# Optimization experiments

Hardware: AMD Instinct MI355X
Metric: run time of the kernel (lower is better)

The kernel has to match this reference:

```python
import jax, jax.numpy as jnp
from jax import lax
import numpy as np

H = 512        # hidden_state_dim
D = 300        # embedding dim (data.x.shape[1])
VG = 40000     # n globals = last_idx_globals - last_idx_senses
VS = 25000     # n senses  = last_idx_senses
NNODES = 65000 # rows of X (senses + globals)
T = 1024       # flattened token sequence length


def setup_inputs() -> dict:
    key = jax.random.key(0)
    ks = jax.random.split(key, 18)
    s = 0.05
    w = lambda k, shape: (jax.random.normal(k, shape, jnp.float32) * s)
    return {
        "tokens": jax.random.randint(ks[0], (T,), 0, NNODES),
        "X":   w(ks[1], (NNODES, D)),
        "Wz1": w(ks[2], (D, H)), "Uz1": w(ks[3], (H, H)),
        "Wr1": w(ks[4], (D, H)), "Ur1": w(ks[5], (H, H)),
        "W1":  w(ks[6], (D, H)), "U1":  w(ks[7], (H, H)),
        "Wz2": w(ks[8], (H, H)), "Uz2": w(ks[9], (H, H)),
        "Wr2": w(ks[10], (H, H)), "Ur2": w(ks[11], (H, H)),
        "W2":  w(ks[12], (H, H)), "U2":  w(ks[13], (H, H)),
        "Wg":  w(ks[14], (H, VG)), "bg": jnp.zeros((VG,), jnp.float32),
        "Ws":  w(ks[15], (H, VS)), "bs": jnp.zeros((VS,), jnp.float32),
    }


def reference(tokens, X, Wz1, Uz1, Wr1, Ur1, W1, U1,
              Wz2, Uz2, Wr2, Ur2, W2, U2, Wg, bg, Ws, bs):
    # Embedding gather for the whole sequence up front (same math as
    # per-step index_select). Dropout (p=0.1) treated as eval/identity.
    x_emb = X[tokens]                       # [T, D]
    h = Uz1.shape[0]
    h0 = jnp.zeros((h,), X.dtype)

    def step(carry, x):
        h1, h2 = carry
        # layer-1 GRU cell
        z1 = jax.nn.sigmoid(x @ Wz1 + h1 @ Uz1)
        r1 = jax.nn.sigmoid(x @ Wr1 + h1 @ Ur1)
        ht1 = jnp.tanh(x @ W1 + (r1 * h1) @ U1)
        h1n = z1 * ht1 + (1.0 - z1) * h1
        # layer-2 GRU cell
        z2 = jax.nn.sigmoid(h1n @ Wz2 + h2 @ Uz2)
        r2 = jax.nn.sigmoid(h1n @ Wr2 + h2 @ Ur2)
        ht2 = jnp.tanh(h1n @ W2 + (r2 * h2) @ U2)
        h2n = z2 * ht2 + (1.0 - z2) * h2
        return (h1n, h2n), h2n

    _, h2s = lax.scan(step, (h0, h0), x_emb)   # h2s: [T, H]

    # vocab projections + log-softmax, batched over all tokens
    pred_globals = jax.nn.log_softmax(h2s @ Wg + bg, axis=-1)  # [T, VG]
    pred_senses = jax.nn.log_softmax(h2s @ Ws + bs, axis=-1)   # [T, VS]
    return pred_globals, pred_senses
```

## Files before the change

### kernel.cpp

```cpp
#include <hip/hip_runtime.h>
#include <stdint.h>

typedef unsigned short u16;
typedef unsigned int u32;
typedef unsigned long long u64;

#define Hdim 512
#define Ddim 300
#define Tlen 1024
#define VG 40000
#define VS 25000
#define NGTOT (Tlen * VG)
#define NTOT  (Tlen * (VG + VS))

#define F_XZ   0
#define F_XR   (F_XZ + Tlen * Hdim)
#define F_X1   (F_XR + Tlen * Hdim)
#define F_H1X  (F_X1 + Tlen * Hdim)
#define F_H2X  (F_H1X + (Tlen + 1) * Hdim * 2)
#define F_R1X  (F_H2X + (Tlen + 1) * Hdim * 2)
#define F_R2X  (F_R1X + Tlen * Hdim * 2)
#define F_HBF  (F_R2X + Tlen * Hdim * 2)
#define F_WGBF (F_HBF + (Tlen * Hdim) / 2)
#define F_WSBF (F_WGBF + (Hdim * VG) / 2)
#define F_PG   (F_WSBF + (Hdim * VS) / 2)
#define F_PS   (F_PG + Tlen * 625)
#define F_LSE  (F_PS + Tlen * 391)

__device__ __forceinline__ u16 f2bf(float f) {
    u32 u = __float_as_uint(f);
    u += 0x7fffu + ((u >> 16) & 1u);
    return (u16)(u >> 16);
}
__device__ __forceinline__ float bf2f(u16 s) { return __uint_as_float(((u32)s) << 16); }
__device__ __forceinline__ float sigm(float x) { return 1.f / (1.f + __expf(-x)); }

__device__ __forceinline__ u64 pk(u32 tag, float v) {
    return ((u64)tag << 32) | (u64)__float_as_uint(v);
}
__device__ __forceinline__ float upf(u64 x) { return __uint_as_float((u32)x); }
__device__ __forceinline__ u32 uptag(u64 x) { return (u32)(x >> 32); }
__device__ __forceinline__ u64 ld64(const u64* p) {
    return __hip_atomic_load(p, __ATOMIC_RELAXED, __HIP_MEMORY_SCOPE_AGENT);
}
__device__ __forceinline__ void st64(u64* p, u64 v) {
    __hip_atomic_store(p, v, __ATOMIC_RELAXED, __HIP_MEMORY_SCOPE_AGENT);
}
__device__ __forceinline__ u64 spin64(const u64* p, u32 tg) {
    u64 a = ld64(p);
    while (uptag(a) != tg) { __builtin_amdgcn_s_sleep(1); a = ld64(p); }
    return a;
}

__global__ void k_init(u64* h1x, u64* h2x) {
    int i = blockIdx.x * 256 + threadIdx.x;
    if (i < Hdim) { h1x[i] = pk(1u, 0.f); h2x[i] = pk(1u, 0.f); }
}

__launch_bounds__(256)
__global__ void k_xproj(const int* tokens, const float* X,
                        const float* Wz1, const float* Wr1, const float* W1,
                        float* xz, float* xr, float* x1) {
    int tid = threadIdx.x;
    int jj = tid & 63, tg = tid >> 6;
    int mat = blockIdx.y >> 3;
    int j0 = (blockIdx.y & 7) * 64;
    int t0 = blockIdx.x * 16 + tg * 4;
    const float* W = (mat == 0) ? Wz1 : (mat == 1 ? Wr1 : W1);
    float* out = (mat == 0) ? xz : (mat == 1 ? xr : x1);
    const float* xrow[4];
#pragma unroll
    for (int u = 0; u < 4; ++u) xrow[u] = X + (size_t)tokens[t0 + u] * Ddim;
    float acc[4] = {0.f, 0.f, 0.f, 0.f};
    for (int k = 0; k < Ddim; ++k) {
        float w = W[(size_t)k * Hdim + j0 + jj];
#pragma unroll
        for (int u = 0; u < 4; ++u) acc[u] += xrow[u][k] * w;
    }
#pragma unroll
    for (int u = 0; u < 4; ++u) out[(size_t)(t0 + u) * Hdim + j0 + jj] = acc[u];
}

__global__ void k_wconv(const float* Wg, const float* Ws, u16* wgbf, u16* wsbf) {
    const int n4g = (Hdim * VG) / 4;
    const int n4s = (Hdim * VS) / 4;
    int stride = gridDim.x * blockDim.x;
    for (int i = blockIdx.x * blockDim.x + threadIdx.x; i < n4g + n4s; i += stride) {
        float4 v;
        u64* dst;
        if (i < n4g) { v = ((const float4*)Wg)[i]; dst = (u64*)wgbf + i; }
        else { int j = i - n4g; v = ((const float4*)Ws)[j]; dst = (u64*)wsbf + j; }
        u64 p = (u64)f2bf(v.x) | ((u64)f2bf(v.y) << 16) | ((u64)f2bf(v.z) << 32) | ((u64)f2bf(v.w) << 48);
        *dst = p;
    }
}

__global__ void k_hbf(const u64* h2x, u16* hbf) {
    int i = blockIdx.x * 256 + threadIdx.x;
    hbf[i] = f2bf(upf(ld64(&h2x[i + Hdim])));
}

#define G1n 32
#define C1n 16
#define G2n 64
#define C2n 8
#define WS 516

__launch_bounds__(256)
__global__ void k_scan(const float* Uz1, const float* Ur1, const float* U1,
                       const float* Wz2, const float* Uz2, const float* Wr2,
                       const float* Ur2, const float* W2, const float* U2,
                       const float* xz, const float* xr, const float* x1,
                       u64* h1x, u64* h2x, u64* r1x, u64* r2x) {
    __shared__ u16 wsl[48 * WS];
    __shared__ float hA[2][Hdim], hB[2][Hdim], hC[2][Hdim];
    int tid = threadIdx.x;
    int g = blockIdx.x;

    if (g < G1n) {
        int c0 = g * C1n;
        const float* Us[3] = {Uz1, Ur1, U1};
        for (int m = 0; m < 3; ++m) {
            for (int k = 0; k < 2; ++k) {
                int i = tid + k * 256;
                const float* src = Us[m] + (size_t)i * Hdim + c0;
                float v[16];
#pragma unroll
                for (int q = 0; q < 4; ++q) {
                    float4 f = ((const float4*)src)[q];
                    v[q * 4] = f.x; v[q * 4 + 1] = f.y; v[q * 4 + 2] = f.z; v[q * 4 + 3] = f.w;
                }
#pragma unroll
                for (int cc = 0; cc < 16; ++cc) wsl[(m * C1n + cc) * WS + i] = f2bf(v[cc]);
            }
        }
        __syncthreads();
        int c = tid >> 4, r = tid & 15;
        const u16* wz = &wsl[(0 * C1n + c) * WS];
        const u16* wr = &wsl[(1 * C1n + c) * WS];
        const u16* w1 = &wsl[(2 * C1n + c) * WS];
        for (int t = 0; t < Tlen; ++t) {
            int p = t & 1;
            float xzv = 0.f, xrv = 0.f, x1v = 0.f;
            if (r == 0) {
                xzv = xz[t * Hdim + c0 + c];
                xrv = xr[t * Hdim + c0 + c];
                x1v = x1[t * Hdim + c0 + c];
            }
            {
                const u64* ph = h1x + (size_t)t * Hdim;
                u32 tg = (u32)(t + 1);
                u64 a0 = spin64(ph + tid, tg);
                u64 a1 = spin64(ph + tid + 256, tg);
                hA[p][tid] = upf(a0); hA[p][tid + 256] = upf(a1);
            }
            __syncthreads();
            float ar = 0.f;
#pragma unroll 8
            for (int ii = 0; ii < 32; ++ii) {
                int i = r * 32 + ((ii + r) & 31);
                ar += hA[p][i] * bf2f(wr[i]);
            }
#pragma unroll
            for (int d = 8; d; d >>= 1) ar += __shfl_down(ar, d, 16);
            if (r == 0) {
                float rg = sigm(ar + xrv);
                st64(&r1x[(size_t)t * Hdim + c0 + c], pk((u32)(t + 1), rg));
            }
            float az = 0.f;
            float pm[32];
#pragma unroll
            for (int ii = 0; ii < 32; ++ii) {
                int i = r * 32 + ((ii + r) & 31);
                float h = hA[p][i];
                az += h * bf2f(wz[i]);
                pm[ii] = h * bf2f(w1[i]);
            }
#pragma unroll
            for (int d = 8; d; d >>= 1) az += __shfl_down(az, d, 16);
            float zg = 0.f;
            if (r == 0) zg = sigm(az + xzv);
            {
                const u64* pr = r1x + (size_t)t * Hdim;
                u32 tg = (u32)(t + 1);
                u64 a0 = spin64(pr + tid, tg);
                u64 a1 = spin64(pr + tid + 256, tg);
                hB[p][tid] = upf(a0); hB[p][tid + 256] = upf(a1);
            }
            __syncthreads();
            float a = 0.f;
#pragma unroll
            for (int ii = 0; ii < 32; ++ii) {
                int i = r * 32 + ((ii + r) & 31);
                a += hB[p][i] * pm[ii];
            }
#pragma unroll
            for (int d = 8; d; d >>= 1) a += __shfl_down(a, d, 16);
            if (r == 0) {
                float ht = tanhf(a + x1v);
                float hn = zg * ht + (1.f - zg) * hA[p][c0 + c];
                st64(&h1x[(size_t)(t + 1) * Hdim + c0 + c], pk((u32)(t + 2), hn));
            }
        }
    } else {
        int g2 = g - G1n, c0 = g2 * C2n;
        const float* Us[6] = {Wz2, Uz2, Wr2, Ur2, W2, U2};
        for (int m = 0; m < 6; ++m) {
            for (int k = 0; k < 2; ++k) {
                int i = tid + k * 256;
                const float* src = Us[m] + (size_t)i * Hdim + c0;
                float v[8];
#pragma unroll
                for (int q = 0; q < 2; ++q) {
                    float4 f = ((const float4*)src)[q];
                    v[q * 4] = f.x; v[q * 4 + 1] = f.y; v[q * 4 + 2] = f.z; v[q * 4 + 3] = f.w;
                }
#pragma unroll
                for (int cc = 0; cc < 8; ++cc) wsl[(m * C2n + cc) * WS + i] = f2bf(v[cc]);
            }
        }
        __syncthreads();
        int c = tid >> 5, r = tid & 31;
        const u16* w0 = &wsl[(0 * C2n + c) * WS];
        const u16* w1p = &wsl[(1 * C2n + c) * WS];
        const u16* w2p = &wsl[(2 * C2n + c) * WS];
        const u16* w3p = &wsl[(3 * C2n + c) * WS];
        const u16* w4p = &wsl[(4 * C2n + c) * WS];
        const u16* w5p = &wsl[(5 * C2n + c) * WS];
        for (int t = 0; t < Tlen; ++t) {
            int p = t & 1;
            {
                const u64* p1 = h1x + (size_t)(t + 1) * Hdim;
                const u64* p2 = h2x + (size_t)t * Hdim;
                u32 tg1 = (u32)(t + 2), tg2 = (u32)(t + 1);
                u64 a0 = spin64(p1 + tid, tg1);
                u64 a1 = spin64(p1 + tid + 256, tg1);
                u64 b0 = spin64(p2 + tid, tg2);
                u64 b1 = spin64(p2 + tid + 256, tg2);
                hA[p][tid] = upf(a0); hA[p][tid + 256] = upf(a1);
                hB[p][tid] = upf(b0); hB[p][tid + 256] = upf(b1);
            }
            __syncthreads();
            float ar = 0.f;
#pragma unroll 8
            for (int ii = 0; ii < 16; ++ii) {
                int i = r * 16 + ((ii + r) & 15);
                ar += hA[p][i] * bf2f(w2p[i]) + hB[p][i] * bf2f(w3p[i]);
            }
#pragma unroll
            for (int d = 16; d; d >>= 1) ar += __shfl_down(ar, d, 32);
            if (r == 0) {
                st64(&r2x[(size_t)t * Hdim + c0 + c], pk((u32)(t + 1), sigm(ar)));
            }
            float az = 0.f, ap = 0.f;
            float pm[16];
#pragma unroll
            for (int ii = 0; ii < 16; ++ii) {
                int i = r * 16 + ((ii + r) & 15);
                float a_ = hA[p][i], b_ = hB[p][i];
                az += a_ * bf2f(w0[i]) + b_ * bf2f(w1p[i]);
                ap += a_ * bf2f(w4p[i]);
                pm[ii] = b_ * bf2f(w5p[i]);
            }
#pragma unroll
            for (int d = 16; d; d >>= 1) az += __shfl_down(az, d, 32);
            float zg = 0.f;
            if (r == 0) zg = sigm(az);
            {
                const u64* pr = r2x + (size_t)t * Hdim;
                u32 tg = (u32)(t + 1);
                u64 a0 = spin64(pr + tid, tg);
                u64 a1 = spin64(pr + tid + 256, tg);
                hC[p][tid] = upf(a0); hC[p][tid + 256] = upf(a1);
            }
            __syncthreads();
            float a = ap;
#pragma unroll
            for (int ii = 0; ii < 16; ++ii) {
                int i = r * 16 + ((ii + r) & 15);
                a += hC[p][i] * pm[ii];
            }
#pragma unroll
            for (int d = 16; d; d >>= 1) a += __shfl_down(a, d, 32);
            if (r == 0) {
                float ht = tanhf(a);
                float hn = zg * ht + (1.f - zg) * hB[p][c0 + c];
                st64(&h2x[(size_t)(t + 1) * Hdim + c0 + c], pk((u32)(t + 2), hn));
            }
        }
    }
}

typedef __attribute__((ext_vector_type(8))) short bfrag;
typedef __attribute__((ext_vector_type(4))) float f32x4;

__launch_bounds__(256)
__global__ void k_gemm(const u16* A, const u16* B, const float* bias,
                       float* out, float* partial, int N, int nblk) {
    __shared__ u16 As[64 * 40];
    __shared__ u16 Bs[64 * 40];
    int tid = threadIdx.x, lane = tid & 63, wid = tid >> 6;
    int m0 = blockIdx.x * 64, n0 = blockIdx.y * 64;
    f32x4 acc[4] = {{0.f, 0.f, 0.f, 0.f}, {0.f, 0.f, 0.f, 0.f}, {0.f, 0.f, 0.f, 0.f}, {0.f, 0.f, 0.f, 0.f}};
    int arow = tid >> 2, akc = (tid & 3) * 8;
    int bkr = tid >> 3, bnc = (tid & 7) * 8;
    bool bvalid = (n0 + bnc) < N;
    int lm = lane & 15, q = lane >> 4;
    for (int kt = 0; kt < 16; ++kt) {
        int k0 = kt * 32;
        uint4 av = *(const uint4*)(A + (size_t)(m0 + arow) * Hdim + k0 + akc);
        *((uint4*)&As[arow * 40 + akc]) = av;
        union { uint4 v; u16 s[8]; } ub;
        ub.v = make_uint4(0, 0, 0, 0);
        if (bvalid) ub.v = *(const uint4*)(B + (size_t)(k0 + bkr) * N + n0 + bnc);
#pragma unroll
        for (int j = 0; j < 8; ++j) Bs[(bnc + j) * 40 + bkr] = ub.s[j];
        __syncthreads();
        bfrag af = *(const bfrag*)&As[(wid * 16 + lm) * 40 + q * 8];
#pragma unroll
        for (int ns = 0; ns < 4; ++ns) {
            bfrag bf_ = *(const bfrag*)&Bs[(ns * 16 + lm) * 40 + q * 8];
            acc[ns] = __builtin_amdgcn_mfma_f32_16x16x32_bf16(af, bf_, acc[ns], 0, 0, 0);
        }
        __syncthreads();
    }
    float rs[4] = {0.f, 0.f, 0.f, 0.f};
#pragma unroll
    for (int ns = 0; ns < 4; ++ns) {
        int col = n0 + ns * 16 + lm;
        bool cv = col < N;
        float bi = cv ? bias[col] : 0.f;
#pragma unroll
        for (int rr = 0; rr < 4; ++rr) {
            int row = wid * 16 + q * 4 + rr;
            float v = acc[ns][rr] + bi;
            if (cv) {
                out[(size_t)(m0 + row) * N + col] = v;
                rs[rr] += __expf(v);
            }
        }
    }
#pragma unroll
    for (int rr = 0; rr < 4; ++rr) {
#pragma unroll
        for (int d = 1; d < 16; d <<= 1) rs[rr] += __shfl_xor(rs[rr], d, 64);
    }
    if (lm == 0) {
#pragma unroll
        for (int rr = 0; rr < 4; ++rr) {
            int row = wid * 16 + q * 4 + rr;
            partial[(size_t)(m0 + row) * nblk + blockIdx.y] = rs[rr];
        }
    }
}

__global__ void k_lse(const float* pG, const float* pS, float* lse) {
    int row = blockIdx.x;
    int tid = threadIdx.x;
    const float* p;
    int nb;
    if (row < Tlen) { p = pG + (size_t)row * 625; nb = 625; }
    else { p = pS + (size_t)(row - Tlen) * 391; nb = 391; }
    float s = 0.f;
    for (int j = tid; j < nb; j += 256) s += p[j];
#pragma unroll
    for (int d = 32; d; d >>= 1) s += __shfl_down(s, d, 64);
    __shared__ float red[4];
    if ((tid & 63) == 0) red[tid >> 6] = s;
    __syncthreads();
    if (tid == 0) lse[row] = logf(red[0] + red[1] + red[2] + red[3]);
}

__global__ void k_fix(float* out, const float* lse) {
    const size_t n4 = NTOT / 4;
    size_t stride = (size_t)gridDim.x * blockDim.x;
    for (size_t i = (size_t)blockIdx.x * blockDim.x + threadIdx.x; i < n4; i += stride) {
        size_t e = i * 4;
        float l;
        if (e < (size_t)NGTOT) l = lse[e / VG];
        else l = lse[Tlen + (e - (size_t)NGTOT) / VS];
        float4 v = ((float4*)out)[i];
        v.x -= l; v.y -= l; v.z -= l; v.w -= l;
        ((float4*)out)[i] = v;
    }
}

extern "C" void kernel_launch(void* const* d_in, const int* in_sizes, int n_in,
                              void* d_out, int out_size, void* d_ws, size_t ws_size,
                              hipStream_t stream) {
    const int* tokens = (const int*)d_in[0];
    const float* X   = (const float*)d_in[1];
    const float* Wz1 = (const float*)d_in[2];
    const float* Uz1 = (const float*)d_in[3];
    const float* Wr1 = (const float*)d_in[4];
    const float* Ur1 = (const float*)d_in[5];
    const float* W1  = (const float*)d_in[6];
    const float* U1  = (const float*)d_in[7];
    const float* Wz2 = (const float*)d_in[8];
    const float* Uz2 = (const float*)d_in[9];
    const float* Wr2 = (const float*)d_in[10];
    const float* Ur2 = (const float*)d_in[11];
    const float* W2  = (const float*)d_in[12];
    const float* U2  = (const float*)d_in[13];
    const float* Wg  = (const float*)d_in[14];
    const float* bg  = (const float*)d_in[15];
    const float* Ws  = (const float*)d_in[16];
    const float* bs  = (const float*)d_in[17];

    float* wsf = (float*)d_ws;
    float* xz = wsf + F_XZ;
    float* xr = wsf + F_XR;
    float* x1 = wsf + F_X1;
    u64* h1x = (u64*)(wsf + F_H1X);
    u64* h2x = (u64*)(wsf + F_H2X);
    u64* r1x = (u64*)(wsf + F_R1X);
    u64* r2x = (u64*)(wsf + F_R2X);
    u16* hbf  = (u16*)(wsf + F_HBF);
    u16* wgbf = (u16*)(wsf + F_WGBF);
    u16* wsbf = (u16*)(wsf + F_WSBF);
    float* pG = wsf + F_PG;
    float* pS = wsf + F_PS;
    float* lse = wsf + F_LSE;
    float* outF = (float*)d_out;

    hipLaunchKernelGGL(k_init, dim3(2), dim3(256), 0, stream, h1x, h2x);
    hipLaunchKernelGGL(k_xproj, dim3(64, 24), dim3(256), 0, stream,
                       tokens, X, Wz1, Wr1, W1, xz, xr, x1);
    hipLaunchKernelGGL(k_wconv, dim3(4096), dim3(256), 0, stream, Wg, Ws, wgbf, wsbf);
    hipLaunchKernelGGL(k_scan, dim3(96), dim3(256), 0, stream,
                       Uz1, Ur1, U1, Wz2, Uz2, Wr2, Ur2, W2, U2,
                       xz, xr, x1, h1x, h2x, r1x, r2x);
    hipLaunchKernelGGL(k_hbf, dim3(2048), dim3(256), 0, stream, h2x, hbf);
    hipLaunchKernelGGL(k_gemm, dim3(16, 625), dim3(256), 0, stream,
                       hbf, wgbf, bg, outF, pG, VG, 625);
    hipLaunchKernelGGL(k_gemm, dim3(16, 391), dim3(256), 0, stream,
                       hbf, wsbf, bs, outF + (size_t)NGTOT, pS, VS, 391);
    hipLaunchKernelGGL(k_lse, dim3(2048), dim3(256), 0, stream, pG, pS, lse);
    hipLaunchKernelGGL(k_fix, dim3(8192), dim3(256), 0, stream, outF, lse);
}
```

Baseline: 5.702 ms.

## Replace per-element tagged spin-waits with per-wavefront release flags in GRU scan

Each recurrent sync point in the persistent scan kernel used to spin on every tagged 64-bit hidden-state element. Now each producing wavefront publishes a release flag once its values are written, and consumers poll a compact flag array, then do an acquire fence and re-read only elements whose tag is still stale. Data loads are issued before the flag wait so their latency overlaps the wait. This aims to cut per-step polling traffic on the serial critical path, at the cost of extra flag stores, fences and workspace.

```diff
diff --git a/kernel.cpp b/kernel.cpp
--- a/kernel.cpp
+++ b/kernel.cpp
@@ -26,6 +26,10 @@
 #define F_PG   (F_WSBF + (Hdim * VS) / 2)
 #define F_PS   (F_PG + Tlen * 625)
 #define F_LSE  (F_PS + Tlen * 391)
+#define F_DH1  (F_LSE + 2048)
+#define F_DR1  (F_DH1 + (Tlen + 1) * 128)
+#define F_DH2  (F_DR1 + Tlen * 128)
+#define F_DR2  (F_DH2 + (Tlen + 1) * 256)
 
 __device__ __forceinline__ u16 f2bf(float f) {
     u32 u = __float_as_uint(f);
@@ -46,15 +50,19 @@
 __device__ __forceinline__ void st64(u64* p, u64 v) {
     __hip_atomic_store(p, v, __ATOMIC_RELAXED, __HIP_MEMORY_SCOPE_AGENT);
 }
-__device__ __forceinline__ u64 spin64(const u64* p, u32 tg) {
-    u64 a = ld64(p);
-    while (uptag(a) != tg) { __builtin_amdgcn_s_sleep(1); a = ld64(p); }
-    return a;
-}
-
-__global__ void k_init(u64* h1x, u64* h2x) {
+__device__ __forceinline__ void stflag(u32* p, u32 v) {
+    __hip_atomic_store(p, v, __ATOMIC_RELEASE, __HIP_MEMORY_SCOPE_AGENT);
+}
+__device__ __forceinline__ void waitflag(const u32* p, u32 tg) {
+    while (__hip_atomic_load(p, __ATOMIC_RELAXED, __HIP_MEMORY_SCOPE_AGENT) != tg)
+        __builtin_amdgcn_s_sleep(1);
+}
+
+__global__ void k_init(u64* h1x, u64* h2x, u32* dh1, u32* dh2) {
     int i = blockIdx.x * 256 + threadIdx.x;
     if (i < Hdim) { h1x[i] = pk(1u, 0.f); h2x[i] = pk(1u, 0.f); }
+    if (i < 128) dh1[i] = 1u;
+    if (i < 256) dh2[i] = 1u;
 }
 
 __launch_bounds__(256)
@@ -111,11 +119,13 @@
                        const float* Wz2, const float* Uz2, const float* Wr2,
                        const float* Ur2, const float* W2, const float* U2,
                        const float* xz, const float* xr, const float* x1,
-                       u64* h1x, u64* h2x, u64* r1x, u64* r2x) {
+                       u64* h1x, u64* h2x, u64* r1x, u64* r2x,
+                       u32* dh1, u32* dr1, u32* dh2, u32* dr2) {
     __shared__ u16 wsl[48 * WS];
     __shared__ float hA[2][Hdim], hB[2][Hdim], hC[2][Hdim];
     int tid = threadIdx.x;
     int g = blockIdx.x;
+    int wv = tid >> 6;
 
     if (g < G1n) {
         int c0 = g * C1n;
@@ -141,19 +151,20 @@
         const u16* w1 = &wsl[(2 * C1n + c) * WS];
         for (int t = 0; t < Tlen; ++t) {
             int p = t & 1;
+            u32 tg = (u32)(t + 1);
             float xzv = 0.f, xrv = 0.f, x1v = 0.f;
             if (r == 0) {
                 xzv = xz[t * Hdim + c0 + c];
                 xrv = xr[t * Hdim + c0 + c];
                 x1v = x1[t * Hdim + c0 + c];
             }
-            {
-                const u64* ph = h1x + (size_t)t * Hdim;
-                u32 tg = (u32)(t + 1);
-                u64 a0 = spin64(ph + tid, tg);
-                u64 a1 = spin64(ph + tid + 256, tg);
-                hA[p][tid] = upf(a0); hA[p][tid + 256] = upf(a1);
-            }
+            const u64* ph = h1x + (size_t)t * Hdim;
+            u64 a0 = ld64(ph + tid), a1 = ld64(ph + tid + 256);
+            if (tid < 128) waitflag(dh1 + (size_t)t * 128 + tid, tg);
+            __builtin_amdgcn_fence(__ATOMIC_ACQUIRE, "agent");
+            if (uptag(a0) != tg) a0 = ld64(ph + tid);
+            if (uptag(a1) != tg) a1 = ld64(ph + tid + 256);
+            hA[p][tid] = upf(a0); hA[p][tid + 256] = upf(a1);
             __syncthreads();
             float ar = 0.f;
 #pragma unroll 8
@@ -165,8 +176,11 @@
             for (int d = 8; d; d >>= 1) ar += __shfl_down(ar, d, 16);
             if (r == 0) {
                 float rg = sigm(ar + xrv);
-                st64(&r1x[(size_t)t * Hdim + c0 + c], pk((u32)(t + 1), rg));
-            }
+                st64(&r1x[(size_t)t * Hdim + c0 + c], pk(tg, rg));
+            }
+            if ((tid & 63) == 0) stflag(dr1 + (size_t)t * 128 + g * 4 + wv, tg);
+            const u64* pr = r1x + (size_t)t * Hdim;
+            u64 b0 = ld64(pr + tid), b1 = ld64(pr + tid + 256);
             float az = 0.f;
             float pm[32];
 #pragma unroll
@@ -180,13 +194,11 @@
             for (int d = 8; d; d >>= 1) az += __shfl_down(az, d, 16);
             float zg = 0.f;
             if (r == 0) zg = sigm(az + xzv);
-            {
-                const u64* pr = r1x + (size_t)t * Hdim;
-                u32 tg = (u32)(t + 1);
-                u64 a0 = spin64(pr + tid, tg);
-                u64 a1 = spin64(pr + tid + 256, tg);
-                hB[p][tid] = upf(a0); hB[p][tid + 256] = upf(a1);
-            }
+            if (tid < 128) waitflag(dr1 + (size_t)t * 128 + tid, tg);
+            __builtin_amdgcn_fence(__ATOMIC_ACQUIRE, "agent");
+            if (uptag(b0) != tg) b0 = ld64(pr + tid);
+            if (uptag(b1) != tg) b1 = ld64(pr + tid + 256);
+            hB[p][tid] = upf(b0); hB[p][tid + 256] = upf(b1);
             __syncthreads();
             float a = 0.f;
 #pragma unroll
@@ -201,6 +213,7 @@
                 float hn = zg * ht + (1.f - zg) * hA[p][c0 + c];
                 st64(&h1x[(size_t)(t + 1) * Hdim + c0 + c], pk((u32)(t + 2), hn));
             }
+            if ((tid & 63) == 0) stflag(dh1 + (size_t)(t + 1) * 128 + g * 4 + wv, (u32)(t + 2));
         }
     } else {
         int g2 = g - G1n, c0 = g2 * C2n;
@@ -229,17 +242,20 @@
         const u16* w5p = &wsl[(5 * C2n + c) * WS];
         for (int t = 0; t < Tlen; ++t) {
             int p = t & 1;
-            {
-                const u64* p1 = h1x + (size_t)(t + 1) * Hdim;
-                const u64* p2 = h2x + (size_t)t * Hdim;
-                u32 tg1 = (u32)(t + 2), tg2 = (u32)(t + 1);
-                u64 a0 = spin64(p1 + tid, tg1);
-                u64 a1 = spin64(p1 + tid + 256, tg1);
-                u64 b0 = spin64(p2 + tid, tg2);
-                u64 b1 = spin64(p2 + tid + 256, tg2);
-                hA[p][tid] = upf(a0); hA[p][tid + 256] = upf(a1);
-                hB[p][tid] = upf(b0); hB[p][tid + 256] = upf(b1);
-            }
+            u32 tgA = (u32)(t + 2), tgB = (u32)(t + 1);
+            const u64* p1 = h1x + (size_t)(t + 1) * Hdim;
+            const u64* p2 = h2x + (size_t)t * Hdim;
+            u64 a0 = ld64(p1 + tid), a1 = ld64(p1 + tid + 256);
+            u64 b0 = ld64(p2 + tid), b1 = ld64(p2 + tid + 256);
+            waitflag(dh2 + (size_t)t * 256 + tid, tgB);
+            if (tid < 128) waitflag(dh1 + (size_t)(t + 1) * 128 + tid, tgA);
+            __builtin_amdgcn_fence(__ATOMIC_ACQUIRE, "agent");
+            if (uptag(a0) != tgA) a0 = ld64(p1 + tid);
+            if (uptag(a1) != tgA) a1 = ld64(p1 + tid + 256);
+            if (uptag(b0) != tgB) b0 = ld64(p2 + tid);
+            if (uptag(b1) != tgB) b1 = ld64(p2 + tid + 256);
+            hA[p][tid] = upf(a0); hA[p][tid + 256] = upf(a1);
+            hB[p][tid] = upf(b0); hB[p][tid + 256] = upf(b1);
             __syncthreads();
             float ar = 0.f;
 #pragma unroll 8
@@ -250,8 +266,11 @@
 #pragma unroll
             for (int d = 16; d; d >>= 1) ar += __shfl_down(ar, d, 32);
             if (r == 0) {
-                st64(&r2x[(size_t)t * Hdim + c0 + c], pk((u32)(t + 1), sigm(ar)));
-            }
+                st64(&r2x[(size_t)t * Hdim + c0 + c], pk(tgB, sigm(ar)));
+            }
+            if ((tid & 63) == 0) stflag(dr2 + (size_t)t * 256 + g2 * 4 + wv, tgB);
+            const u64* pr = r2x + (size_t)t * Hdim;
+            u64 c0v = ld64(pr + tid), c1v = ld64(pr + tid + 256);
             float az = 0.f, ap = 0.f;
             float pm[16];
 #pragma unroll
@@ -266,13 +285,11 @@
             for (int d = 16; d; d >>= 1) az += __shfl_down(az, d, 32);
             float zg = 0.f;
             if (r == 0) zg = sigm(az);
-            {
-                const u64* pr = r2x + (size_t)t * Hdim;
-                u32 tg = (u32)(t + 1);
-                u64 a0 = spin64(pr + tid, tg);
-                u64 a1 = spin64(pr + tid + 256, tg);
-                hC[p][tid] = upf(a0); hC[p][tid + 256] = upf(a1);
-            }
+            waitflag(dr2 + (size_t)t * 256 + tid, tgB);
+            __builtin_amdgcn_fence(__ATOMIC_ACQUIRE, "agent");
+            if (uptag(c0v) != tgB) c0v = ld64(pr + tid);
+            if (uptag(c1v) != tgB) c1v = ld64(pr + tid + 256);
+            hC[p][tid] = upf(c0v); hC[p][tid + 256] = upf(c1v);
             __syncthreads();
             float a = ap;
 #pragma unroll
@@ -287,6 +304,7 @@
                 float hn = zg * ht + (1.f - zg) * hB[p][c0 + c];
                 st64(&h2x[(size_t)(t + 1) * Hdim + c0 + c], pk((u32)(t + 2), hn));
             }
+            if ((tid & 63) == 0) stflag(dh2 + (size_t)(t + 1) * 256 + g2 * 4 + wv, (u32)(t + 2));
         }
     }
 }
@@ -421,15 +439,19 @@
     float* pG = wsf + F_PG;
     float* pS = wsf + F_PS;
     float* lse = wsf + F_LSE;
+    u32* dh1 = (u32*)(wsf + F_DH1);
+    u32* dr1 = (u32*)(wsf + F_DR1);
+    u32* dh2 = (u32*)(wsf + F_DH2);
+    u32* dr2 = (u32*)(wsf + F_DR2);
     float* outF = (float*)d_out;
 
-    hipLaunchKernelGGL(k_init, dim3(2), dim3(256), 0, stream, h1x, h2x);
+    hipLaunchKernelGGL(k_init, dim3(2), dim3(256), 0, stream, h1x, h2x, dh1, dh2);
     hipLaunchKernelGGL(k_xproj, dim3(64, 24), dim3(256), 0, stream,
                        tokens, X, Wz1, Wr1, W1, xz, xr, x1);
     hipLaunchKernelGGL(k_wconv, dim3(4096), dim3(256), 0, stream, Wg, Ws, wgbf, wsbf);
     hipLaunchKernelGGL(k_scan, dim3(96), dim3(256), 0, stream,
                        Uz1, Ur1, U1, Wz2, Uz2, Wr2, Ur2, W2, U2,
-                       xz, xr, x1, h1x, h2x, r1x, r2x);
+                       xz, xr, x1, h1x, h2x, r1x, r2x, dh1, dr1, dh2, dr2);
     hipLaunchKernelGGL(k_hbf, dim3(2048), dim3(256), 0, stream, h2x, hbf);
     hipLaunchKernelGGL(k_gemm, dim3(16, 625), dim3(256), 0, stream,
                        hbf, wgbf, bg, outF, pG, VG, 625);
```

New measurement: 19.90 ms. 249% more time.

## Halve scan workgroups, widen column slices, and batch spin-wait flag polling

Applied to the files above, without the earlier changes.

Cuts the persistent GRU scan from 96 to 48 workgroups, each owning twice as many hidden columns, so fewer workgroups join each cross-workgroup flag handoff. Spin-waiting now polls two adjacent tagged slots per thread together and starts the r-gate flag load early, so it overlaps with the z-gate dot product. The pm register array is dropped in favour of recomputing h*w inside the third dot product. In exchange, each workgroup does twice the per-step dot-product work serially, which lengthens the per-step critical path.

```diff
diff --git a/kernel.cpp b/kernel.cpp
--- a/kernel.cpp
+++ b/kernel.cpp
@@ -46,10 +46,13 @@
 __device__ __forceinline__ void st64(u64* p, u64 v) {
     __hip_atomic_store(p, v, __ATOMIC_RELAXED, __HIP_MEMORY_SCOPE_AGENT);
 }
-__device__ __forceinline__ u64 spin64(const u64* p, u32 tg) {
-    u64 a = ld64(p);
-    while (uptag(a) != tg) { __builtin_amdgcn_s_sleep(1); a = ld64(p); }
-    return a;
+
+__device__ __forceinline__ void spinpair(const u64* q, u32 tg, u64& a0, u64& a1) {
+    while (uptag(a0) != tg || uptag(a1) != tg) {
+        __builtin_amdgcn_s_sleep(2);
+        if (uptag(a0) != tg) a0 = ld64(q);
+        if (uptag(a1) != tg) a1 = ld64(q + 1);
+    }
 }
 
 __global__ void k_init(u64* h1x, u64* h2x) {
@@ -100,10 +103,10 @@
     hbf[i] = f2bf(upf(ld64(&h2x[i + Hdim])));
 }
 
-#define G1n 32
-#define C1n 16
-#define G2n 64
-#define C2n 8
+#define G1n 16
+#define C1n 32
+#define G2n 32
+#define C2n 16
 #define WS 516
 
 __launch_bounds__(256)
@@ -112,10 +115,11 @@
                        const float* Ur2, const float* W2, const float* U2,
                        const float* xz, const float* xr, const float* x1,
                        u64* h1x, u64* h2x, u64* r1x, u64* r2x) {
-    __shared__ u16 wsl[48 * WS];
+    __shared__ u16 wsl[96 * WS];
     __shared__ float hA[2][Hdim], hB[2][Hdim], hC[2][Hdim];
     int tid = threadIdx.x;
     int g = blockIdx.x;
+    int s0 = tid * 2, s1 = tid * 2 + 1;
 
     if (g < G1n) {
         int c0 = g * C1n;
@@ -124,23 +128,24 @@
             for (int k = 0; k < 2; ++k) {
                 int i = tid + k * 256;
                 const float* src = Us[m] + (size_t)i * Hdim + c0;
-                float v[16];
-#pragma unroll
-                for (int q = 0; q < 4; ++q) {
+#pragma unroll
+                for (int q = 0; q < 8; ++q) {
                     float4 f = ((const float4*)src)[q];
-                    v[q * 4] = f.x; v[q * 4 + 1] = f.y; v[q * 4 + 2] = f.z; v[q * 4 + 3] = f.w;
+                    wsl[(m * C1n + q * 4 + 0) * WS + i] = f2bf(f.x);
+                    wsl[(m * C1n + q * 4 + 1) * WS + i] = f2bf(f.y);
+                    wsl[(m * C1n + q * 4 + 2) * WS + i] = f2bf(f.z);
+                    wsl[(m * C1n + q * 4 + 3) * WS + i] = f2bf(f.w);
                 }
-#pragma unroll
-                for (int cc = 0; cc < 16; ++cc) wsl[(m * C1n + cc) * WS + i] = f2bf(v[cc]);
             }
         }
         __syncthreads();
-        int c = tid >> 4, r = tid & 15;
+        int c = tid >> 3, r = tid & 7;
         const u16* wz = &wsl[(0 * C1n + c) * WS];
         const u16* wr = &wsl[(1 * C1n + c) * WS];
         const u16* w1 = &wsl[(2 * C1n + c) * WS];
         for (int t = 0; t < Tlen; ++t) {
             int p = t & 1;
+            u32 tg = (u32)(t + 1);
             float xzv = 0.f, xrv = 0.f, x1v = 0.f;
             if (r == 0) {
                 xzv = xz[t * Hdim + c0 + c];
@@ -149,53 +154,46 @@
             }
             {
                 const u64* ph = h1x + (size_t)t * Hdim;
-                u32 tg = (u32)(t + 1);
-                u64 a0 = spin64(ph + tid, tg);
-                u64 a1 = spin64(ph + tid + 256, tg);
-                hA[p][tid] = upf(a0); hA[p][tid + 256] = upf(a1);
+                u64 a0 = ld64(ph + s0), a1 = ld64(ph + s1);
+                spinpair(ph + s0, tg, a0, a1);
+                hA[p][s0] = upf(a0); hA[p][s1] = upf(a1);
             }
             __syncthreads();
             float ar = 0.f;
 #pragma unroll 8
-            for (int ii = 0; ii < 32; ++ii) {
-                int i = r * 32 + ((ii + r) & 31);
+            for (int ii = 0; ii < 64; ++ii) {
+                int i = r * 64 + ((ii + r) & 63);
                 ar += hA[p][i] * bf2f(wr[i]);
             }
 #pragma unroll
-            for (int d = 8; d; d >>= 1) ar += __shfl_down(ar, d, 16);
+            for (int d = 4; d; d >>= 1) ar += __shfl_down(ar, d, 8);
             if (r == 0) {
                 float rg = sigm(ar + xrv);
-                st64(&r1x[(size_t)t * Hdim + c0 + c], pk((u32)(t + 1), rg));
-            }
+                st64(&r1x[(size_t)t * Hdim + c0 + c], pk(tg, rg));
+            }
+            const u64* pr = r1x + (size_t)t * Hdim;
+            u64 b0 = ld64(pr + s0), b1 = ld64(pr + s1);
             float az = 0.f;
-            float pm[32];
-#pragma unroll
-            for (int ii = 0; ii < 32; ++ii) {
-                int i = r * 32 + ((ii + r) & 31);
-                float h = hA[p][i];
-                az += h * bf2f(wz[i]);
-                pm[ii] = h * bf2f(w1[i]);
-            }
-#pragma unroll
-            for (int d = 8; d; d >>= 1) az += __shfl_down(az, d, 16);
+#pragma unroll 8
+            for (int ii = 0; ii < 64; ++ii) {
+                int i = r * 64 + ((ii + r) & 63);
+                az += hA[p][i] * bf2f(wz[i]);
+            }
+#pragma unroll
+            for (int d = 4; d; d >>= 1) az += __shfl_down(az, d, 8);
             float zg = 0.f;
             if (r == 0) zg = sigm(az + xzv);
-            {
-                const u64* pr = r1x + (size_t)t * Hdim;
-                u32 tg = (u32)(t + 1);
-                u64 a0 = spin64(pr + tid, tg);
-                u64 a1 = spin64(pr + tid + 256, tg);
-                hB[p][tid] = upf(a0); hB[p][tid + 256] = upf(a1);
-            }
+            spinpair(pr + s0, tg, b0, b1);
+            hB[p][s0] = upf(b0); hB[p][s1] = upf(b1);
             __syncthreads();
             float a = 0.f;
-#pragma unroll
-            for (int ii = 0; ii < 32; ++ii) {
-                int i = r * 32 + ((ii + r) & 31);
-                a += hB[p][i] * pm[ii];
-            }
-#pragma unroll
-            for (int d = 8; d; d >>= 1) a += __shfl_down(a, d, 16);
+#pragma unroll 8
+            for (int ii = 0; ii < 64; ++ii) {
+                int i = r * 64 + ((ii + r) & 63);
+                a += hB[p][i] * hA[p][i] * bf2f(w1[i]);
+            }
+#pragma unroll
+            for (int d = 4; d; d >>= 1) a += __shfl_down(a, d, 8);
             if (r == 0) {
                 float ht = tanhf(a + x1v);
                 float hn = zg * ht + (1.f - zg) * hA[p][c0 + c];
@@ -209,18 +207,18 @@
             for (int k = 0; k < 2; ++k) {
                 int i = tid + k * 256;
                 const float* src = Us[m] + (size_t)i * Hdim + c0;
-                float v[8];
-#pragma unroll
-                for (int q = 0; q < 2; ++q) {
+#pragma unroll
+                for (int q = 0; q < 4; ++q) {
                     float4 f = ((const float4*)src)[q];
-                    v[q * 4] = f.x; v[q * 4 + 1] = f.y; v[q * 4 + 2] = f.z; v[q * 4 + 3] = f.w;
+                    wsl[(m * C2n + q * 4 + 0) * WS + i] = f2bf(f.x);
+                    wsl[(m * C2n + q * 4 + 1) * WS + i] = f2bf(f.y);
+                    wsl[(m * C2n + q * 4 + 2) * WS + i] = f2bf(f.z);
+                    wsl[(m * C2n + q * 4 + 3) * WS + i] = f2bf(f.w);
                 }
-#pragma unroll
-                for (int cc = 0; cc < 8; ++cc) wsl[(m * C2n + cc) * WS + i] = f2bf(v[cc]);
             }
         }
         __syncthreads();
-        int c = tid >> 5, r = tid & 31;
+        int c = tid >> 4, r = tid & 15;
         const u16* w0 = &wsl[(0 * C2n + c) * WS];
         const u16* w1p = &wsl[(1 * C2n + c) * WS];
         const u16* w2p = &wsl[(2 * C2n + c) * WS];
@@ -229,59 +227,60 @@
         const u16* w5p = &wsl[(5 * C2n + c) * WS];
         for (int t = 0; t < Tlen; ++t) {
             int p = t & 1;
+            u32 tgA = (u32)(t + 2), tgB = (u32)(t + 1);
             {
                 const u64* p1 = h1x + (size_t)(t + 1) * Hdim;
                 const u64* p2 = h2x + (size_t)t * Hdim;
-                u32 tg1 = (u32)(t + 2), tg2 = (u32)(t + 1);
-                u64 a0 = spin64(p1 + tid, tg1);
-                u64 a1 = spin64(p1 + tid + 256, tg1);
-                u64 b0 = spin64(p2 + tid, tg2);
-                u64 b1 = spin64(p2 + tid + 256, tg2);
-                hA[p][tid] = upf(a0); hA[p][tid + 256] = upf(a1);
-                hB[p][tid] = upf(b0); hB[p][tid + 256] = upf(b1);
+                u64 a0 = ld64(p1 + s0), a1 = ld64(p1 + s1);
+                u64 b0 = ld64(p2 + s0), b1 = ld64(p2 + s1);
+                while (uptag(a0) != tgA || uptag(a1) != tgA ||
+                       uptag(b0) != tgB || uptag(b1) != tgB) {
+                    __builtin_amdgcn_s_sleep(2);
+                    if (uptag(a0) != tgA) a0 = ld64(p1 + s0);
+                    if (uptag(a1) != tgA) a1 = ld64(p1 + s1);
+                    if (uptag(b0) != tgB) b0 = ld64(p2 + s0);
+                    if (uptag(b1) != tgB) b1 = ld64(p2 + s1);
+                }
+                hA[p][s0] = upf(a0); hA[p][s1] = upf(a1);
+                hB[p][s0] = upf(b0); hB[p][s1] = upf(b1);
             }
             __syncthreads();
             float ar = 0.f;
 #pragma unroll 8
-            for (int ii = 0; ii < 16; ++ii) {
-                int i = r * 16 + ((ii + r) & 15);
+            for (int ii = 0; ii < 32; ++ii) {
+                int i = r * 32 + ((ii + r) & 31);
                 ar += hA[p][i] * bf2f(w2p[i]) + hB[p][i] * bf2f(w3p[i]);
             }
 #pragma unroll
-            for (int d = 16; d; d >>= 1) ar += __shfl_down(ar, d, 32);
+            for (int d = 8; d; d >>= 1) ar += __shfl_down(ar, d, 16);
             if (r == 0) {
-                st64(&r2x[(size_t)t * Hdim + c0 + c], pk((u32)(t + 1), sigm(ar)));
-            }
+                st64(&r2x[(size_t)t * Hdim + c0 + c], pk(tgB, sigm(ar)));
+            }
+            const u64* pr = r2x + (size_t)t * Hdim;
+            u64 cb0 = ld64(pr + s0), cb1 = ld64(pr + s1);
             float az = 0.f, ap = 0.f;
-            float pm[16];
-#pragma unroll
-            for (int ii = 0; ii < 16; ++ii) {
-                int i = r * 16 + ((ii + r) & 15);
+#pragma unroll 8
+            for (int ii = 0; ii < 32; ++ii) {
+                int i = r * 32 + ((ii + r) & 31);
                 float a_ = hA[p][i], b_ = hB[p][i];
                 az += a_ * bf2f(w0[i]) + b_ * bf2f(w1p[i]);
                 ap += a_ * bf2f(w4p[i]);
-                pm[ii] = b_ * bf2f(w5p[i]);
-            }
-#pragma unroll
-            for (int d = 16; d; d >>= 1) az += __shfl_down(az, d, 32);
+            }
+#pragma unroll
+            for (int d = 8; d; d >>= 1) az += __shfl_down(az, d, 16);
             float zg = 0.f;
             if (r == 0) zg = sigm(az);
-            {
-                const u64* pr = r2x + (size_t)t * Hdim;
-                u32 tg = (u32)(t + 1);
-                u64 a0 = spin64(pr + tid, tg);
-                u64 a1 = spin64(pr + tid + 256, tg);
-                hC[p][tid] = upf(a0); hC[p][tid + 256] = upf(a1);
-            }
+            spinpair(pr + s0, tgB, cb0, cb1);
+            hC[p][s0] = upf(cb0); hC[p][s1] = upf(cb1);
             __syncthreads();
             float a = ap;
-#pragma unroll
-            for (int ii = 0; ii < 16; ++ii) {
-                int i = r * 16 + ((ii + r) & 15);
-                a += hC[p][i] * pm[ii];
-            }
-#pragma unroll
-            for (int d = 16; d; d >>= 1) a += __shfl_down(a, d, 32);
+#pragma unroll 8
+            for (int ii = 0; ii < 32; ++ii) {
+                int i = r * 32 + ((ii + r) & 31);
+                a += hC[p][i] * hB[p][i] * bf2f(w5p[i]);
+            }
+#pragma unroll
+            for (int d = 8; d; d >>= 1) a += __shfl_down(a, d, 16);
             if (r == 0) {
                 float ht = tanhf(a);
                 float hn = zg * ht + (1.f - zg) * hB[p][c0 + c];
@@ -427,7 +426,7 @@
     hipLaunchKernelGGL(k_xproj, dim3(64, 24), dim3(256), 0, stream,
                        tokens, X, Wz1, Wr1, W1, xz, xr, x1);
     hipLaunchKernelGGL(k_wconv, dim3(4096), dim3(256), 0, stream, Wg, Ws, wgbf, wsbf);
-    hipLaunchKernelGGL(k_scan, dim3(96), dim3(256), 0, stream,
+    hipLaunchKernelGGL(k_scan, dim3(G1n + G2n), dim3(256), 0, stream,
                        Uz1, Ur1, U1, Wz2, Uz2, Wr2, Ur2, W2, U2,
                        xz, xr, x1, h1x, h2x, r1x, r2x);
     hipLaunchKernelGGL(k_hbf, dim3(2048), dim3(256), 0, stream, h2x, hbf);
```

Result: slower. 8.204 ms (+43.9%).
